# Optimization experiments

Measured on AMD Instinct MI355X. Metric: run time of the kernel, lower is better.

Reference implementation:

```python
import jax, jax.numpy as jnp
import numpy as np

N, K, D = 65536, 1024, 256


def setup_inputs() -> dict:
    key = jax.random.key(0)
    k1, k2 = jax.random.split(key)
    e = jax.random.normal(k1, (N, D), dtype=jnp.float32)
    # module inits codebook uniform in [-1/K, 1/K]
    weight = jax.random.uniform(k2, (K, D), dtype=jnp.float32,
                                minval=-1.0 / K, maxval=1.0 / K)
    return {"e": e, "weight": weight}


def reference(e, weight):
    distances = (jnp.sum(e * e, axis=1, keepdims=True)
                 - 2.0 * jnp.matmul(e, weight.T)
                 + jnp.sum(weight * weight, axis=1))
    encoding_indices = jnp.argmin(distances, axis=1)            # [N]
    # one-hot @ weight is just a gather
    quantized = weight[encoding_indices]                        # [N, D]
    commitment_loss = jnp.mean((jax.lax.stop_gradient(quantized) - e) ** 2)
    counts = jnp.zeros((K,), dtype=jnp.float32).at[encoding_indices].add(1.0)
    codebook_usage = counts.max() / counts.sum()
    # straight-through estimator
    quantized = e + jax.lax.stop_gradient(quantized - e)
    return quantized, encoding_indices, commitment_loss, codebook_usage
```

## Files before the change

kernel.cpp:

```cpp
#include <hip/hip_runtime.h>

typedef __attribute__((ext_vector_type(8))) short short8;
typedef __attribute__((ext_vector_type(4))) float floatx4;

#define N_ROWS 65536
#define K_CB   1024
#define D_DIM  256

#define TAU 3.0e-4f
#define BLINE 520

#define OFF_RN     0
#define OFF_WN     262144
#define OFF_FIXCNT 266240
#define OFF_HIST   266496
#define OFF_IDX    270592
#define OFF_LIST   532736
#define OFF_PART   794880
#define OFF_WFRAG  827392
#define OFF_KEYS   1351680

__device__ __forceinline__ float pw128_sq(const float4* p) {
#pragma clang fp contract(off)
    float4 q0 = p[0], q1 = p[1];
    float r0 = q0.x * q0.x, r1 = q0.y * q0.y, r2 = q0.z * q0.z, r3 = q0.w * q0.w;
    float r4 = q1.x * q1.x, r5 = q1.y * q1.y, r6 = q1.z * q1.z, r7 = q1.w * q1.w;
    for (int i = 1; i < 16; ++i) {
        float4 u0 = p[2 * i], u1 = p[2 * i + 1];
        r0 = r0 + u0.x * u0.x; r1 = r1 + u0.y * u0.y;
        r2 = r2 + u0.z * u0.z; r3 = r3 + u0.w * u0.w;
        r4 = r4 + u1.x * u1.x; r5 = r5 + u1.y * u1.y;
        r6 = r6 + u1.z * u1.z; r7 = r7 + u1.w * u1.w;
    }
    return ((r0 + r1) + (r2 + r3)) + ((r4 + r5) + (r6 + r7));
}
__device__ __forceinline__ float rownorm_np(const float* row) {
#pragma clang fp contract(off)
    float s0 = pw128_sq((const float4*)row);
    float s1 = pw128_sq((const float4*)(row + 128));
    return s0 + s1;
}
__device__ __forceinline__ float np_dist(float A, float m, float Ck) {
#pragma clang fp contract(off)
    float Bv = 2.0f * m;
    float t  = A - Bv;
    return t + Ck;
}
__device__ __forceinline__ unsigned short bf16_rne(float x) {
    unsigned u = __float_as_uint(x);
    unsigned r = u + 0x7fff + ((u >> 16) & 1);
    return (unsigned short)(r >> 16);
}
__device__ __forceinline__ float bf16_tof(unsigned short h) {
    return __uint_as_float(((unsigned)h) << 16);
}

#define PRS 260
__global__ __launch_bounds__(256) void k_prep(
        const float* __restrict__ eg, const float* __restrict__ wg,
        float* __restrict__ rn, float* __restrict__ wn,
        unsigned short* __restrict__ wfrag) {
    __shared__ __align__(16) float es[32 * PRS];
    const int tid = threadIdx.x;
    const int bx  = blockIdx.x;
    if (bx < 2048) {
        const int rowBase = bx * 32;
        #pragma unroll
        for (int j = 0; j < 8; ++j) {
            int f4 = j * 256 + tid;
            int row = f4 >> 6, k4 = f4 & 63;
            float4 v = *(const float4*)(eg + (size_t)(rowBase + row) * D_DIM + k4 * 4);
            *(float4*)&es[row * PRS + k4 * 4] = v;
        }
        __syncthreads();
        if (tid < 64) {
            int row = tid >> 1, half = tid & 1;
            float s = pw128_sq((const float4*)&es[row * PRS + half * 128]);
            float so = __shfl_xor(s, 1, 64);
            if (half == 0) rn[rowBase + row] = s + so;
        }
    } else if (bx < 2052) {
        int row = (bx - 2048) * 256 + tid;
        wn[row] = rownorm_np(wg + (size_t)row * D_DIM);
    } else {
        int t = (bx - 2052) * 256 + tid;
        int col = t >> 5, kc = t & 31;
        const float4* src = (const float4*)(wg + (size_t)col * D_DIM + kc * 8);
        float4 v0 = src[0], v1 = src[1];
        const float a[8] = {v0.x, v0.y, v0.z, v0.w, v1.x, v1.y, v1.z, v1.w};
        short8 h;
        #pragma unroll
        for (int i = 0; i < 8; ++i) h[i] = (short)bf16_rne(a[i]);
        *(short8*)(wfrag + ((size_t)kc * 1024 + col) * 8) = h;
    }
}

__global__ __launch_bounds__(256, 4) void k_dist(
        const float* __restrict__ eg, const unsigned short* __restrict__ wfrag,
        const float* __restrict__ wn,
        int* __restrict__ idx_ws, int* __restrict__ fixlist, int* __restrict__ fixcnt) {
    __shared__ __align__(16) unsigned short Bs[32 * BLINE];
    __shared__ float wnS[K_CB];
    const int tid  = threadIdx.x;
    const int lane = tid & 63;
    const int wv   = tid >> 6;
    const int q    = lane >> 4;
    const int m15  = lane & 15;
    const int waveRow = blockIdx.x * 64 + wv * 16;

    #pragma unroll
    for (int i = 0; i < 4; ++i) wnS[tid + i * 256] = wn[tid + i * 256];

    short8 afh[8], afl[8];
    {
        const float* rowp = eg + (size_t)(waveRow + m15) * D_DIM + q * 8;
        #pragma unroll
        for (int win = 0; win < 8; ++win) {
            const float4* pa = (const float4*)(rowp + win * 32);
            float4 x0 = pa[0], x1 = pa[1];
            const float a[8] = {x0.x, x0.y, x0.z, x0.w, x1.x, x1.y, x1.z, x1.w};
            short8 h, l;
            #pragma unroll
            for (int i = 0; i < 8; ++i) {
                unsigned short hh = bf16_rne(a[i]);
                h[i] = (short)hh;
                l[i] = (short)bf16_rne(a[i] - bf16_tof(hh));
            }
            afh[win] = h;
            afl[win] = l;
        }
    }

    float best[4], sec[4];
    int bidx[4];
    #pragma unroll
    for (int s = 0; s < 4; ++s) { best[s] = 3.4e38f; sec[s] = 3.4e38f; bidx[s] = 0; }

    for (int cb = 0; cb < 16; ++cb) {
        __syncthreads();
        #pragma unroll
        for (int t = 0; t < 8; ++t) {
            int L = wv * 8 + t;
            const unsigned short* src = wfrag + ((size_t)L * 1024 + cb * 64) * 8 + lane * 8;
            __builtin_amdgcn_global_load_lds(
                (const __attribute__((address_space(1))) unsigned int*)src,
                (__attribute__((address_space(3))) unsigned int*)&Bs[L * BLINE],
                16, 0, 0);
        }
        __syncthreads();

        floatx4 acc[4];
        #pragma unroll
        for (int nt = 0; nt < 4; ++nt)
            acc[nt] = (floatx4){0.f, 0.f, 0.f, 0.f};

        #pragma unroll
        for (int nt = 0; nt < 4; ++nt) {
            #pragma unroll
            for (int win = 0; win < 8; ++win) {
                int kc = win * 4 + q;
                short8 bfh = *(short8*)&Bs[kc * BLINE + (nt * 16 + m15) * 8];
                acc[nt] = __builtin_amdgcn_mfma_f32_16x16x32_bf16(afh[win], bfh, acc[nt], 0, 0, 0);
                acc[nt] = __builtin_amdgcn_mfma_f32_16x16x32_bf16(afl[win], bfh, acc[nt], 0, 0, 0);
            }
        }
        #pragma unroll
        for (int nt = 0; nt < 4; ++nt) {
            int col = cb * 64 + nt * 16 + m15;
            float Ck = wnS[col];
            #pragma unroll
            for (int reg = 0; reg < 4; ++reg) {
                float d = __builtin_fmaf(-2.0f, acc[nt][reg], Ck);
                bool lt = d < best[reg];
                sec[reg]  = __builtin_amdgcn_fmed3f(d, best[reg], sec[reg]);
                best[reg] = fminf(d, best[reg]);
                bidx[reg] = lt ? col : bidx[reg];
            }
        }
    }

    #pragma unroll
    for (int s = 0; s < 4; ++s) {
        float b = best[s], se = sec[s];
        int ix = bidx[s];
        #pragma unroll
        for (int m = 1; m < 16; m <<= 1) {
            float bo = __shfl_xor(b, m, 64);
            float so = __shfl_xor(se, m, 64);
            int   io = __shfl_xor(ix, m, 64);
            float ns = fminf(fminf(se, so), fmaxf(b, bo));
            if (bo < b || (bo == b && io < ix)) { b = bo; ix = io; }
            se = ns;
        }
        if (m15 == 0) {
            int row = waveRow + q * 4 + s;
            idx_ws[row] = ix;
            if (se - b < TAU) {
                int p = atomicAdd(fixcnt, 1);
                fixlist[p] = row;
            }
        }
    }
}

#define FG_ROWS 8
__global__ __launch_bounds__(256) void k_fixup(
        const float* __restrict__ eg, const float* __restrict__ wg,
        const float* __restrict__ rn, const float* __restrict__ wnorm,
        const int* __restrict__ fixlist, const int* __restrict__ fixcnt,
        unsigned long long* __restrict__ keys) {
    __shared__ double xs[FG_ROWS][D_DIM];
    const int tid = threadIdx.x;
    const int cnt = *fixcnt;
    if (cnt == 0) return;
    const int ngroups = (cnt + FG_ROWS - 1) / FG_ROWS;
    const int ntiles  = ngroups * 4;
    for (int t = blockIdx.x; t < ntiles; t += gridDim.x) {
        const int g     = t >> 2;
        const int chunk = t & 3;
        __syncthreads();
        int rows[FG_ROWS];
        #pragma unroll
        for (int i = 0; i < FG_ROWS; ++i) {
            int j = g * FG_ROWS + i;
            rows[i] = fixlist[j < cnt ? j : cnt - 1];
        }
        #pragma unroll
        for (int i = 0; i < FG_ROWS; ++i)
            xs[i][tid] = (double)eg[(size_t)rows[i] * D_DIM + tid];
        __syncthreads();
        float An[FG_ROWS];
        #pragma unroll
        for (int i = 0; i < FG_ROWS; ++i) An[i] = rn[rows[i]];

        const int k = chunk * 256 + tid;
        const float4* wr = (const float4*)(wg + (size_t)k * D_DIM);
        double s[FG_ROWS];
        #pragma unroll
        for (int i = 0; i < FG_ROWS; ++i) s[i] = 0.0;
        for (int i = 0; i < D_DIM / 4; ++i) {
            float4 f = wr[i];
            double f0 = f.x, f1 = f.y, f2 = f.z, f3 = f.w;
            #pragma unroll
            for (int r = 0; r < FG_ROWS; ++r)
                s[r] += xs[r][4*i] * f0 + xs[r][4*i+1] * f1
                      + xs[r][4*i+2] * f2 + xs[r][4*i+3] * f3;
        }
        const float Cw = wnorm[k];
        #pragma unroll
        for (int r = 0; r < FG_ROWS; ++r) {
            float d = np_dist(An[r], (float)s[r], Cw);
            unsigned u = __float_as_uint(d);
            unsigned key32 = u ^ (((unsigned)((int)u >> 31)) | 0x80000000u);
            unsigned long long key = ((unsigned long long)key32 << 32) | (unsigned)k;
            #pragma unroll
            for (int m = 1; m < 64; m <<= 1) {
                unsigned long long o = __shfl_xor(key, m, 64);
                key = (o < key) ? o : key;
            }
            int j = g * FG_ROWS + r;
            if ((tid & 63) == 0 && j < cnt) atomicMin(&keys[j], key);
        }
    }
}

__global__ void k_fixscatter(const int* __restrict__ fixlist, const int* __restrict__ fixcnt,
                             const unsigned long long* __restrict__ keys,
                             int* __restrict__ idx_ws) {
    const int cnt = *fixcnt;
    for (int j = blockIdx.x * blockDim.x + threadIdx.x; j < cnt;
         j += gridDim.x * blockDim.x)
        idx_ws[fixlist[j]] = (int)(keys[j] & 0xFFFFFFFFull);
}

__global__ void k_final(const float* __restrict__ eg, const float* __restrict__ wg,
                        const int* __restrict__ idx_ws, float* __restrict__ qout,
                        float* __restrict__ iout, int* __restrict__ hist,
                        double* __restrict__ partials) {
    const int tid  = threadIdx.x;
    const int sub  = tid >> 6;
    const int lane = tid & 63;
    const int rowBase = blockIdx.x * 16;
    double acc = 0.0;
    #pragma unroll
    for (int g = 0; g < 4; ++g) {
        int row = rowBase + g * 4 + sub;
        int k = idx_ws[row];
        float4 ev = ((const float4*)(eg + (size_t)row * D_DIM))[lane];
        float4 wv = ((const float4*)(wg + (size_t)k   * D_DIM))[lane];
        float dx = wv.x - ev.x, dy = wv.y - ev.y, dz = wv.z - ev.z, dw = wv.w - ev.w;
        float4 qv = {ev.x + dx, ev.y + dy, ev.z + dz, ev.w + dw};
        ((float4*)(qout + (size_t)row * D_DIM))[lane] = qv;
        acc += (double)(dx * dx) + (double)(dy * dy)
             + (double)(dz * dz) + (double)(dw * dw);
        if (lane == 0) {
            iout[row] = (float)k;
            atomicAdd(&hist[k], 1);
        }
    }
    __shared__ double red[256];
    red[tid] = acc;
    __syncthreads();
    for (int st = 128; st > 0; st >>= 1) {
        if (tid < st) red[tid] += red[tid + st];
        __syncthreads();
    }
    if (tid == 0) partials[blockIdx.x] = red[0];
}

__global__ void k_scalars(const int* __restrict__ hist, const double* __restrict__ partials,
                          float* __restrict__ sout) {
    const int tid = threadIdx.x;
    double s = 0.0;
    for (int j = tid; j < N_ROWS / 16; j += 256) s += partials[j];
    int m = 0;
    for (int j = tid; j < K_CB; j += 256) m = max(m, hist[j]);
    __shared__ double rs[256];
    __shared__ int    rm[256];
    rs[tid] = s; rm[tid] = m;
    __syncthreads();
    for (int st = 128; st > 0; st >>= 1) {
        if (tid < st) { rs[tid] += rs[tid + st]; rm[tid] = max(rm[tid], rm[tid + st]); }
        __syncthreads();
    }
    if (tid == 0) {
        sout[0] = (float)(rs[0] / (double)((size_t)N_ROWS * D_DIM));
        sout[1] = (float)rm[0] / 65536.0f;
    }
}

extern "C" void kernel_launch(void* const* d_in, const int* in_sizes, int n_in,
                              void* d_out, int out_size, void* d_ws, size_t ws_size,
                              hipStream_t stream) {
    const float* e = (const float*)d_in[0];
    const float* w = (const float*)d_in[1];
    float* out  = (float*)d_out;
    float* qout = out;
    float* iout = out + (size_t)N_ROWS * D_DIM;
    float* sout = iout + N_ROWS;

    char* ws = (char*)d_ws;
    float*  rn       = (float*) (ws + OFF_RN);
    float*  wn       = (float*) (ws + OFF_WN);
    int*    fixcnt   = (int*)   (ws + OFF_FIXCNT);
    int*    hist     = (int*)   (ws + OFF_HIST);
    int*    idxp     = (int*)   (ws + OFF_IDX);
    int*    list     = (int*)   (ws + OFF_LIST);
    double* partials = (double*)(ws + OFF_PART);
    unsigned short* wfrag = (unsigned short*)(ws + OFF_WFRAG);
    unsigned long long* keys = (unsigned long long*)(ws + OFF_KEYS);

    hipMemsetAsync(ws + OFF_FIXCNT, 0, 4352, stream);
    hipMemsetAsync(ws + OFF_KEYS, 0xFF, 524288, stream);

    hipLaunchKernelGGL(k_prep,       dim3(2180),        dim3(256), 0, stream, e, w, rn, wn, wfrag);
    hipLaunchKernelGGL(k_dist,       dim3(1024),        dim3(256), 0, stream, e, wfrag, wn, idxp, list, fixcnt);
    hipLaunchKernelGGL(k_fixup,      dim3(2048),        dim3(256), 0, stream, e, w, rn, wn, list, fixcnt, keys);
    hipLaunchKernelGGL(k_fixscatter, dim3(64),          dim3(256), 0, stream, list, fixcnt, keys, idxp);
    hipLaunchKernelGGL(k_final,      dim3(N_ROWS / 16), dim3(256), 0, stream, e, w, idxp, qout, iout, hist, partials);
    hipLaunchKernelGGL(k_scalars,    dim3(1),           dim3(256), 0, stream, hist, partials, sout);
}
```

Baseline: 363.7 us.

## Transpose codebook in prep and register-tile fp64 fixup as 4x4 blocks

Adds an extra stage to the prep kernel that writes a transposed fp32 copy of the codebook (D x K) to workspace. The fp64 fixup kernel now gives each thread a 4-row by 4-code register tile, reading coalesced float4 columns of the transposed codebook and double2 pairs of cached rows from shared memory. Previously each thread streamed a whole codebook row, uncoalesced across lanes. This improves global coalescing and reuse of each loaded value, but changes the fp64 summation order and costs an extra transpose pass plus 1 MB of workspace.

```diff
diff --git a/kernel.cpp b/kernel.cpp
--- a/kernel.cpp
+++ b/kernel.cpp
@@ -19,6 +19,7 @@
 #define OFF_PART   794880
 #define OFF_WFRAG  827392
 #define OFF_KEYS   1351680
+#define OFF_WT     1875968
 
 __device__ __forceinline__ float pw128_sq(const float4* p) {
 #pragma clang fp contract(off)
@@ -59,7 +60,7 @@
 __global__ __launch_bounds__(256) void k_prep(
         const float* __restrict__ eg, const float* __restrict__ wg,
         float* __restrict__ rn, float* __restrict__ wn,
-        unsigned short* __restrict__ wfrag) {
+        unsigned short* __restrict__ wfrag, float* __restrict__ wt) {
     __shared__ __align__(16) float es[32 * PRS];
     const int tid = threadIdx.x;
     const int bx  = blockIdx.x;
@@ -82,7 +83,7 @@
     } else if (bx < 2052) {
         int row = (bx - 2048) * 256 + tid;
         wn[row] = rownorm_np(wg + (size_t)row * D_DIM);
-    } else {
+    } else if (bx < 2180) {
         int t = (bx - 2052) * 256 + tid;
         int col = t >> 5, kc = t & 31;
         const float4* src = (const float4*)(wg + (size_t)col * D_DIM + kc * 8);
@@ -92,6 +93,24 @@
         #pragma unroll
         for (int i = 0; i < 8; ++i) h[i] = (short)bf16_rne(a[i]);
         *(short8*)(wfrag + ((size_t)kc * 1024 + col) * 8) = h;
+    } else {
+        float (*tw)[PRS] = (float(*)[PRS])es;
+        const int cb = bx - 2180;
+        const int c0 = cb * 32;
+        #pragma unroll
+        for (int it = 0; it < 8; ++it) {
+            int idx = it * 256 + tid;
+            int code = idx >> 6, f4 = idx & 63;
+            *(float4*)&tw[code][f4 * 4] =
+                *(const float4*)(wg + (size_t)(c0 + code) * D_DIM + f4 * 4);
+        }
+        __syncthreads();
+        const int j = tid & 31, dg = tid >> 5;
+        #pragma unroll
+        for (int dd = 0; dd < 32; ++dd) {
+            int d = dd * 8 + dg;
+            wt[(size_t)d * K_CB + c0 + j] = tw[j][d];
+        }
     }
 }
 
@@ -205,7 +224,7 @@
 
 #define FG_ROWS 8
 __global__ __launch_bounds__(256) void k_fixup(
-        const float* __restrict__ eg, const float* __restrict__ wg,
+        const float* __restrict__ eg, const float* __restrict__ wt,
         const float* __restrict__ rn, const float* __restrict__ wnorm,
         const int* __restrict__ fixlist, const int* __restrict__ fixcnt,
         unsigned long long* __restrict__ keys) {
@@ -214,10 +233,12 @@
     const int cnt = *fixcnt;
     if (cnt == 0) return;
     const int ngroups = (cnt + FG_ROWS - 1) / FG_ROWS;
-    const int ntiles  = ngroups * 4;
+    const int ntiles  = ngroups * 2;
+    const int rowg = tid >> 7;
+    const int cg   = tid & 127;
     for (int t = blockIdx.x; t < ntiles; t += gridDim.x) {
-        const int g     = t >> 2;
-        const int chunk = t & 3;
+        const int g     = t >> 1;
+        const int chunk = t & 1;
         __syncthreads();
         int rows[FG_ROWS];
         #pragma unroll
@@ -229,36 +250,54 @@
         for (int i = 0; i < FG_ROWS; ++i)
             xs[i][tid] = (double)eg[(size_t)rows[i] * D_DIM + tid];
         __syncthreads();
-        float An[FG_ROWS];
-        #pragma unroll
-        for (int i = 0; i < FG_ROWS; ++i) An[i] = rn[rows[i]];
-
-        const int k = chunk * 256 + tid;
-        const float4* wr = (const float4*)(wg + (size_t)k * D_DIM);
-        double s[FG_ROWS];
-        #pragma unroll
-        for (int i = 0; i < FG_ROWS; ++i) s[i] = 0.0;
-        for (int i = 0; i < D_DIM / 4; ++i) {
-            float4 f = wr[i];
-            double f0 = f.x, f1 = f.y, f2 = f.z, f3 = f.w;
-            #pragma unroll
-            for (int r = 0; r < FG_ROWS; ++r)
-                s[r] += xs[r][4*i] * f0 + xs[r][4*i+1] * f1
-                      + xs[r][4*i+2] * f2 + xs[r][4*i+3] * f3;
-        }
-        const float Cw = wnorm[k];
-        #pragma unroll
-        for (int r = 0; r < FG_ROWS; ++r) {
-            float d = np_dist(An[r], (float)s[r], Cw);
-            unsigned u = __float_as_uint(d);
-            unsigned key32 = u ^ (((unsigned)((int)u >> 31)) | 0x80000000u);
-            unsigned long long key = ((unsigned long long)key32 << 32) | (unsigned)k;
+
+        const int c0 = chunk * 512 + cg * 4;
+        float An[4];
+        #pragma unroll
+        for (int r = 0; r < 4; ++r) An[r] = rn[rows[rowg * 4 + r]];
+        float Cw[4];
+        #pragma unroll
+        for (int c = 0; c < 4; ++c) Cw[c] = wnorm[c0 + c];
+
+        double s[4][4];
+        #pragma unroll
+        for (int r = 0; r < 4; ++r)
+            #pragma unroll
+            for (int c = 0; c < 4; ++c) s[r][c] = 0.0;
+
+        #pragma unroll 2
+        for (int d = 0; d < D_DIM; d += 2) {
+            float4 wa = *(const float4*)(wt + (size_t)d * K_CB + c0);
+            float4 wb = *(const float4*)(wt + (size_t)(d + 1) * K_CB + c0);
+            double wad[4] = {(double)wa.x, (double)wa.y, (double)wa.z, (double)wa.w};
+            double wbd[4] = {(double)wb.x, (double)wb.y, (double)wb.z, (double)wb.w};
+            #pragma unroll
+            for (int r = 0; r < 4; ++r) {
+                double2 e2 = *(const double2*)&xs[rowg * 4 + r][d];
+                #pragma unroll
+                for (int c = 0; c < 4; ++c)
+                    s[r][c] += e2.x * wad[c] + e2.y * wbd[c];
+            }
+        }
+
+        #pragma unroll
+        for (int r = 0; r < 4; ++r) {
+            unsigned long long key = 0xFFFFFFFFFFFFFFFFull;
+            #pragma unroll
+            for (int c = 0; c < 4; ++c) {
+                float dq = np_dist(An[r], (float)s[r][c], Cw[c]);
+                unsigned u = __float_as_uint(dq);
+                unsigned key32 = u ^ (((unsigned)((int)u >> 31)) | 0x80000000u);
+                unsigned long long kk =
+                    ((unsigned long long)key32 << 32) | (unsigned)(c0 + c);
+                key = kk < key ? kk : key;
+            }
             #pragma unroll
             for (int m = 1; m < 64; m <<= 1) {
                 unsigned long long o = __shfl_xor(key, m, 64);
                 key = (o < key) ? o : key;
             }
-            int j = g * FG_ROWS + r;
+            int j = g * FG_ROWS + rowg * 4 + r;
             if ((tid & 63) == 0 && j < cnt) atomicMin(&keys[j], key);
         }
     }
@@ -349,13 +388,14 @@
     double* partials = (double*)(ws + OFF_PART);
     unsigned short* wfrag = (unsigned short*)(ws + OFF_WFRAG);
     unsigned long long* keys = (unsigned long long*)(ws + OFF_KEYS);
+    float*  wt       = (float*) (ws + OFF_WT);
 
     hipMemsetAsync(ws + OFF_FIXCNT, 0, 4352, stream);
     hipMemsetAsync(ws + OFF_KEYS, 0xFF, 524288, stream);
 
-    hipLaunchKernelGGL(k_prep,       dim3(2180),        dim3(256), 0, stream, e, w, rn, wn, wfrag);
+    hipLaunchKernelGGL(k_prep,       dim3(2212),        dim3(256), 0, stream, e, w, rn, wn, wfrag, wt);
     hipLaunchKernelGGL(k_dist,       dim3(1024),        dim3(256), 0, stream, e, wfrag, wn, idxp, list, fixcnt);
-    hipLaunchKernelGGL(k_fixup,      dim3(2048),        dim3(256), 0, stream, e, w, rn, wn, list, fixcnt, keys);
+    hipLaunchKernelGGL(k_fixup,      dim3(2048),        dim3(256), 0, stream, e, wt, rn, wn, list, fixcnt, keys);
     hipLaunchKernelGGL(k_fixscatter, dim3(64),          dim3(256), 0, stream, list, fixcnt, keys, idxp);
     hipLaunchKernelGGL(k_final,      dim3(N_ROWS / 16), dim3(256), 0, stream, e, w, idxp, qout, iout, hist, partials);
     hipLaunchKernelGGL(k_scalars,    dim3(1),           dim3(256), 0, stream, hist, partials, sout);
```

Result: faster. 347.1 us (-4.6%).
